# Kernel optimization log

Hardware: AMD Instinct MI355X
Metric: run time of the kernel (lower is better)

Reference implementation:

```python
import jax, jax.numpy as jnp
import numpy as np

N = 50000      # nodes
E = 800000     # edges
F_IN = 64      # n_features
H = 128        # graph_hidden_layers
LAT = 128      # latent_size
DH = 1024      # dense_hidden_layers
G = 256        # num graphs in batch
EPS = 1e-5


def setup_inputs() -> dict:
    key = jax.random.key(0)
    ks = jax.random.split(key, 32)
    def rn(k, shape, scale=0.05):
        return jax.random.normal(k, shape, dtype=jnp.float32) * scale
    inp = {
        "x": jax.random.normal(ks[0], (N, F_IN), dtype=jnp.float32),
        "origin": jax.random.normal(ks[1], (G, 3), dtype=jnp.float32),
        "direction": jax.random.normal(ks[2], (G, 3), dtype=jnp.float32),
        "edge_index": jax.random.randint(ks[3], (2, E), 0, N, dtype=jnp.int32),
        "batch": jnp.sort(jax.random.randint(ks[4], (N,), 0, G, dtype=jnp.int32)),
        # GCNConv weights
        "W1": rn(ks[5], (F_IN, H)), "b1": jnp.zeros((H,), jnp.float32),
        "W2": rn(ks[6], (H, H)),    "b2": jnp.zeros((H,), jnp.float32),
        "W3": rn(ks[7], (H, LAT)), "b3": jnp.zeros((LAT,), jnp.float32),
        # BatchNorm affine params
        "g1": jnp.ones((H,), jnp.float32),   "be1": jnp.zeros((H,), jnp.float32),
        "g2": jnp.ones((H,), jnp.float32),   "be2": jnp.zeros((H,), jnp.float32),
        "g3": jnp.ones((LAT,), jnp.float32), "be3": jnp.zeros((LAT,), jnp.float32),
        # Dense head: (LAT+6)->DH, then n_dense_layers=2 of DH->DH, then DH->3
        "Wd0": rn(ks[8], (LAT + 6, DH)), "bd0": jnp.zeros((DH,), jnp.float32),
        "Wd1": rn(ks[9], (DH, DH)),      "bd1": jnp.zeros((DH,), jnp.float32),
        "Wd2": rn(ks[10], (DH, DH)),     "bd2": jnp.zeros((DH,), jnp.float32),
        "Wout": rn(ks[11], (DH, 3)),     "bout": jnp.zeros((3,), jnp.float32),
    }
    return inp


def _gcn_conv(x, W, b, src, dst, deg_inv_sqrt):
    """PyG GCNConv with self-loops: D^{-1/2} (A+I) D^{-1/2} x W + b."""
    xW = x @ W  # [N, out]
    norm = deg_inv_sqrt[src] * deg_inv_sqrt[dst]  # [E]
    msg = xW[src] * norm[:, None]                 # gather + scale
    agg = jax.ops.segment_sum(msg, dst, num_segments=N)
    agg = agg + xW * (deg_inv_sqrt * deg_inv_sqrt)[:, None]  # self-loop term
    return agg + b


def _batchnorm(x, gamma, beta):
    m = jnp.mean(x, axis=0)
    v = jnp.mean(jnp.square(x - m), axis=0)
    return (x - m) * jax.lax.rsqrt(v + EPS) * gamma + beta


def reference(x, origin, direction, edge_index, batch,
              W1, b1, W2, b2, W3, b3,
              g1, be1, g2, be2, g3, be3,
              Wd0, bd0, Wd1, bd1, Wd2, bd2, Wout, bout):
    src, dst = edge_index[0], edge_index[1]
    # degree with self-loops (in-degree at dst, matching gcn_norm)
    deg = jax.ops.segment_sum(jnp.ones((E,), jnp.float32), dst, num_segments=N) + 1.0
    deg_inv_sqrt = jax.lax.rsqrt(deg)

    h = jax.nn.relu(_batchnorm(_gcn_conv(x, W1, b1, src, dst, deg_inv_sqrt), g1, be1))
    h = jax.nn.relu(_batchnorm(_gcn_conv(h, W2, b2, src, dst, deg_inv_sqrt), g2, be2))
    h = _batchnorm(_gcn_conv(h, W3, b3, src, dst, deg_inv_sqrt), g3, be3)

    # global mean pool over graphs
    sums = jax.ops.segment_sum(h, batch, num_segments=G)
    cnt = jax.ops.segment_sum(jnp.ones((N,), jnp.float32), batch, num_segments=G)
    pooled = sums / jnp.maximum(cnt, 1.0)[:, None]  # [G, LAT]

    z = jnp.concatenate([pooled, origin, direction], axis=1)  # [G, LAT+6]
    z = jax.nn.relu(z @ Wd0 + bd0)
    z = jax.nn.relu(z @ Wd1 + bd1)
    z = jax.nn.relu(z @ Wd2 + bd2)
    return z @ Wout + bout  # [G, 3]
```

## Files before the change

kernel.cpp:

```cpp
#include <hip/hip_runtime.h>

#define HC 128
#define FIN 64
#define DHID 1024
#define ZK 134
#define ZKP 160
#define NSCAT 4

typedef __attribute__((ext_vector_type(8))) short short8;
typedef __attribute__((ext_vector_type(8))) __bf16 bf16x8;
typedef __attribute__((ext_vector_type(4))) float f32x4;
typedef __attribute__((ext_vector_type(8))) unsigned short u16x8;
typedef __attribute__((ext_vector_type(4))) unsigned short u16x4;

union FragU { short8 s; bf16x8 b; u16x8 u; };

__device__ inline unsigned short rne_bf16(float x) {
    union { float f; unsigned u; } v; v.f = x;
    unsigned u = v.u;
    unsigned r = (u + 0x7fffu + ((u >> 16) & 1u)) >> 16;
    return (unsigned short)r;
}
__device__ inline float bf16_to_f(unsigned short h) {
    union { unsigned u; float f; } v; v.u = ((unsigned)h) << 16;
    return v.f;
}

__global__ void k_deg_i(const int* __restrict__ dst, int* __restrict__ cnt, int E) {
    int i = blockIdx.x * blockDim.x + threadIdx.x;
    if (i < E) atomicAdd(&cnt[dst[i]], 1);
}

__global__ void k_xtobf(const float* __restrict__ x, unsigned short* __restrict__ xb, int n4) {
    int i = blockIdx.x * blockDim.x + threadIdx.x;
    if (i >= n4) return;
    float4 v = ((const float4*)x)[i];
    u16x4 o;
    o[0] = rne_bf16(v.x); o[1] = rne_bf16(v.y);
    o[2] = rne_bf16(v.z); o[3] = rne_bf16(v.w);
    ((u16x4*)xb)[i] = o;
}

__global__ void k_scan1(const int* __restrict__ cnt, int* __restrict__ part,
                        int* __restrict__ bsum, float* __restrict__ dinv, int N) {
    __shared__ int sh[256];
    int t = threadIdx.x, i = blockIdx.x * 256 + t;
    int v = (i < N) ? cnt[i] : 0;
    if (i < N) dinv[i] = rsqrtf((float)v + 1.0f);
    sh[t] = v; __syncthreads();
    #pragma unroll
    for (int off = 1; off < 256; off <<= 1) {
        int tv = (t >= off) ? sh[t - off] : 0;
        __syncthreads();
        sh[t] += tv;
        __syncthreads();
    }
    if (i < N) part[i] = sh[t] - v;
    if (t == 255) bsum[blockIdx.x] = sh[255];
}

__global__ void k_scan2(int* __restrict__ bsum, int nb) {
    __shared__ int sh[256];
    int t = threadIdx.x;
    int v = (t < nb) ? bsum[t] : 0;
    sh[t] = v; __syncthreads();
    #pragma unroll
    for (int off = 1; off < 256; off <<= 1) {
        int tv = (t >= off) ? sh[t - off] : 0;
        __syncthreads();
        sh[t] += tv;
        __syncthreads();
    }
    if (t < nb) bsum[t] = sh[t] - v;
}

__global__ void k_scan3(const int* __restrict__ part, const int* __restrict__ bsum,
                        int* __restrict__ row_start, int* __restrict__ cur, int N) {
    int i = blockIdx.x * 256 + threadIdx.x;
    if (i < N) { int v = part[i] + bsum[blockIdx.x]; row_start[i] = v; cur[i] = v; }
}

__global__ void k_scatter2(const int* __restrict__ src, const int* __restrict__ dst,
                           const float* __restrict__ dinv,
                           int* __restrict__ cur, int2* __restrict__ csr,
                           int E, int rangeSize) {
    int e = blockIdx.x * blockDim.x + threadIdx.x;
    if (e >= E) return;
    int d = dst[e];
    int lo = blockIdx.y * rangeSize;
    if (d < lo || d >= lo + rangeSize) return;
    int s = src[e];
    int pos = atomicAdd(&cur[d], 1);
    int2 pk; pk.x = s; pk.y = __float_as_int(dinv[s] * dinv[d]);
    csr[pos] = pk;
}

template <int RF> struct BVec;
template <> struct BVec<64>  { using T = u16x4; static const int VPL = 4; };
template <> struct BVec<128> { using T = u16x8; static const int VPL = 8; };

template <int RF>
__global__ __launch_bounds__(256) void k_gather2b(const unsigned short* __restrict__ T,
                                                  const int2* __restrict__ csr,
                                                  const int* __restrict__ row_start,
                                                  const int* __restrict__ cnt,
                                                  const float* __restrict__ dinv,
                                                  unsigned short* __restrict__ agg, int N) {
    using vec = typename BVec<RF>::T;
    constexpr int VPL = BVec<RF>::VPL;
    int tid = threadIdx.x;
    int node = blockIdx.x * 16 + (tid >> 4);
    int q = tid & 15;
    if (node >= N) return;
    int beg = row_start[node];
    int end = beg + cnt[node];
    float d = dinv[node];
    vec sv = ((const vec*)(T + (size_t)node * RF))[q];
    float acc[VPL];
    #pragma unroll
    for (int i = 0; i < VPL; ++i) acc[i] = bf16_to_f(sv[i]) * d * d;
    int j = beg;
    for (; j + 8 <= end; j += 8) {
        int2 e[8];
        #pragma unroll
        for (int u = 0; u < 8; ++u) e[u] = csr[j + u];
        vec v[8];
        #pragma unroll
        for (int u = 0; u < 8; ++u) v[u] = ((const vec*)(T + (size_t)e[u].x * RF))[q];
        #pragma unroll
        for (int u = 0; u < 8; ++u) {
            float nn = __int_as_float(e[u].y);
            #pragma unroll
            for (int i = 0; i < VPL; ++i) acc[i] += bf16_to_f(v[u][i]) * nn;
        }
    }
    for (; j + 2 <= end; j += 2) {
        int2 e0 = csr[j], e1 = csr[j + 1];
        vec v0 = ((const vec*)(T + (size_t)e0.x * RF))[q];
        vec v1 = ((const vec*)(T + (size_t)e1.x * RF))[q];
        float n0 = __int_as_float(e0.y), n1 = __int_as_float(e1.y);
        #pragma unroll
        for (int i = 0; i < VPL; ++i)
            acc[i] += bf16_to_f(v0[i]) * n0 + bf16_to_f(v1[i]) * n1;
    }
    if (j < end) {
        int2 e0 = csr[j];
        vec v0 = ((const vec*)(T + (size_t)e0.x * RF))[q];
        float n0 = __int_as_float(e0.y);
        #pragma unroll
        for (int i = 0; i < VPL; ++i) acc[i] += bf16_to_f(v0[i]) * n0;
    }
    vec o;
    #pragma unroll
    for (int i = 0; i < VPL; ++i) o[i] = rne_bf16(acc[i]);
    ((vec*)(agg + (size_t)node * RF))[q] = o;
}

__global__ __launch_bounds__(256) void k_bn_reduce3(const unsigned short* __restrict__ x,
                                                    float* __restrict__ stat, int N) {
    int cg = threadIdx.x & 15;
    int rr = threadIdx.x >> 4;
    int rpb = (N + gridDim.x - 1) / gridDim.x;
    int r0 = blockIdx.x * rpb;
    int r1 = min(N, r0 + rpb);
    float s0=0.f,s1=0.f,s2=0.f,s3=0.f,s4=0.f,s5=0.f,s6=0.f,s7=0.f;
    float q0=0.f,q1=0.f,q2=0.f,q3=0.f,q4=0.f,q5=0.f,q6=0.f,q7=0.f;
    for (int r = r0 + rr; r < r1; r += 16) {
        u16x8 v = *(const u16x8*)(x + (size_t)r * HC + cg * 8);
        float f;
        f = bf16_to_f(v[0]); s0 += f; q0 += f * f;
        f = bf16_to_f(v[1]); s1 += f; q1 += f * f;
        f = bf16_to_f(v[2]); s2 += f; q2 += f * f;
        f = bf16_to_f(v[3]); s3 += f; q3 += f * f;
        f = bf16_to_f(v[4]); s4 += f; q4 += f * f;
        f = bf16_to_f(v[5]); s5 += f; q5 += f * f;
        f = bf16_to_f(v[6]); s6 += f; q6 += f * f;
        f = bf16_to_f(v[7]); s7 += f; q7 += f * f;
    }
    __shared__ float sh[16][136];
    int c0 = cg * 8;
    int tid = threadIdx.x;
    sh[rr][c0+0]=s0; sh[rr][c0+1]=s1; sh[rr][c0+2]=s2; sh[rr][c0+3]=s3;
    sh[rr][c0+4]=s4; sh[rr][c0+5]=s5; sh[rr][c0+6]=s6; sh[rr][c0+7]=s7;
    __syncthreads();
    if (tid < HC) {
        float tot = 0.f;
        #pragma unroll
        for (int r2 = 0; r2 < 16; ++r2) tot += sh[r2][tid];
        atomicAdd(&stat[tid], tot);
    }
    __syncthreads();
    sh[rr][c0+0]=q0; sh[rr][c0+1]=q1; sh[rr][c0+2]=q2; sh[rr][c0+3]=q3;
    sh[rr][c0+4]=q4; sh[rr][c0+5]=q5; sh[rr][c0+6]=q6; sh[rr][c0+7]=q7;
    __syncthreads();
    if (tid < HC) {
        float tot = 0.f;
        #pragma unroll
        for (int r2 = 0; r2 < 16; ++r2) tot += sh[r2][tid];
        atomicAdd(&stat[HC + tid], tot);
    }
}

__global__ void k_bn_apply3(unsigned short* __restrict__ t, const float* __restrict__ stat,
                            const float* __restrict__ gam, const float* __restrict__ bet,
                            float invN, int total8) {
    int i = blockIdx.x * blockDim.x + threadIdx.x;
    if (i >= total8) return;
    int k0 = (i * 8) & (HC - 1);
    u16x8 v = ((const u16x8*)t)[i];
    u16x8 o;
    #pragma unroll
    for (int j = 0; j < 8; ++j) {
        int k = k0 + j;
        float m = stat[k] * invN;
        float var = stat[HC + k] * invN - m * m;
        float istd = rsqrtf(var + 1e-5f);
        float sc = gam[k] * istd;
        float sh = bet[k] - m * sc;
        o[j] = rne_bf16(fmaxf(bf16_to_f(v[j]) * sc + sh, 0.f));
    }
    ((u16x8*)t)[i] = o;
}

__global__ void k_pool(const unsigned short* __restrict__ h, const int* __restrict__ batch,
                       const float* __restrict__ stat, const float* __restrict__ gam,
                       const float* __restrict__ bet, float invN,
                       float* __restrict__ pooled, float* __restrict__ cnt, int N) {
    int t = threadIdx.x;
    float m = stat[t] * invN;
    float var = stat[HC + t] * invN - m * m;
    float istd = rsqrtf(var + 1e-5f);
    float scv = gam[t] * istd;
    float shv = bet[t] - m * scv;
    int rpb = (N + gridDim.x - 1) / gridDim.x;
    int r0 = blockIdx.x * rpb;
    int r1 = min(N, r0 + rpb);
    if (r0 >= r1) return;
    int curb = batch[r0];
    float acc = 0.f; float c = 0.f;
    for (int r = r0; r < r1; ++r) {
        int b = batch[r];
        if (b != curb) {
            atomicAdd(&pooled[curb * HC + t], acc);
            if (t == 0) atomicAdd(&cnt[curb], c);
            curb = b; acc = 0.f; c = 0.f;
        }
        acc += bf16_to_f(h[(size_t)r * HC + t]) * scv + shv;
        c += 1.f;
    }
    atomicAdd(&pooled[curb * HC + t], acc);
    if (t == 0) atomicAdd(&cnt[curb], c);
}

__global__ void k_build_z(const float* __restrict__ pooled, const float* __restrict__ cnt,
                          const float* __restrict__ origin, const float* __restrict__ dir,
                          float* __restrict__ z, int G) {
    int g = blockIdx.x;
    int t = threadIdx.x;
    if (t >= ZKP) return;
    float v = 0.f;
    if (t < HC) {
        float c = fmaxf(cnt[g], 1.0f);
        v = pooled[g * HC + t] / c;
    } else if (t < HC + 3) {
        v = origin[g * 3 + (t - HC)];
    } else if (t < HC + 6) {
        v = dir[g * 3 + (t - HC - 3)];
    }
    z[g * ZKP + t] = v;
}

__global__ void k_wprep_all(const float* __restrict__ W1, const float* __restrict__ W2,
                            const float* __restrict__ W3,
                            unsigned short* __restrict__ w1h, unsigned short* __restrict__ w1l,
                            unsigned short* __restrict__ w2h, unsigned short* __restrict__ w2l,
                            unsigned short* __restrict__ w3h, unsigned short* __restrict__ w3l) {
    int i = blockIdx.x * blockDim.x + threadIdx.x;
    const float* W; unsigned short *th, *tl; int K, idx;
    if (i < FIN * HC)           { W = W1; th = w1h; tl = w1l; K = FIN; idx = i; }
    else if (i < FIN*HC + HC*HC){ W = W2; th = w2h; tl = w2l; K = HC;  idx = i - FIN*HC; }
    else if (i < FIN*HC + 2*HC*HC){ W = W3; th = w3h; tl = w3l; K = HC; idx = i - FIN*HC - HC*HC; }
    else return;
    int k = idx >> 7, n = idx & (HC - 1);
    float w = W[idx];
    unsigned short h = rne_bf16(w);
    th[n * K + k] = h;
    tl[n * K + k] = rne_bf16(w - bf16_to_f(h));
}

__global__ __launch_bounds__(256) void k_wprep2(const float* __restrict__ W,
                                                unsigned short* __restrict__ th,
                                                unsigned short* __restrict__ tl,
                                                int K, int KP, int NC) {
    __shared__ float tile[32][33];
    int kt = blockIdx.x * 32, nt = blockIdx.y * 32;
    int tx = threadIdx.x & 31, ty0 = threadIdx.x >> 5;
    #pragma unroll
    for (int i = 0; i < 4; ++i) {
        int ty = ty0 + i * 8;
        int k = kt + ty;
        float v = (k < K) ? W[(size_t)k * NC + nt + tx] : 0.f;
        tile[ty][tx] = v;
    }
    __syncthreads();
    #pragma unroll
    for (int i = 0; i < 4; ++i) {
        int ty = ty0 + i * 8;
        int n = nt + ty;
        int k = kt + tx;
        float w = tile[tx][ty];
        unsigned short h = rne_bf16(w);
        th[(size_t)n * KP + k] = h;
        tl[(size_t)n * KP + k] = rne_bf16(w - bf16_to_f(h));
    }
}

template <int KK>
__global__ __launch_bounds__(512) void gemm_node2(const unsigned short* __restrict__ A,
                                                  const unsigned short* __restrict__ wth,
                                                  const unsigned short* __restrict__ wtl,
                                                  unsigned short* __restrict__ C, int M) {
    constexpr int KS = KK / 32;
    int tid = threadIdx.x;
    int lane = tid & 63, wid = tid >> 6;
    int rw = wid & 1, cg = wid >> 1;
    int l15 = lane & 15, l4 = lane >> 4;
    int cbase = cg * 32;

    FragU bh[2][KS], bl[2][KS];
    #pragma unroll
    for (int ct = 0; ct < 2; ++ct) {
        int n = cbase + ct * 16 + l15;
        #pragma unroll
        for (int ks = 0; ks < KS; ++ks) {
            int k = ks * 32 + l4 * 8;
            bh[ct][ks].s = *(const short8*)(wth + (size_t)n * KK + k);
            bl[ct][ks].s = *(const short8*)(wtl + (size_t)n * KK + k);
        }
    }

    #pragma unroll
    for (int rt = 0; rt < 2; ++rt) {
        int m0 = blockIdx.x * 64 + rt * 32 + rw * 16;
        if (m0 < M) {
            int arow = min(m0 + l15, M - 1);
            f32x4 zero = {0.f, 0.f, 0.f, 0.f};
            f32x4 acc[2] = {zero, zero};
            #pragma unroll
            for (int ks = 0; ks < KS; ++ks) {
                int k0 = ks * 32 + l4 * 8;
                FragU a;
                a.u = *(const u16x8*)(A + (size_t)arow * KK + k0);
                #pragma unroll
                for (int ct = 0; ct < 2; ++ct) {
                    acc[ct] = __builtin_amdgcn_mfma_f32_16x16x32_bf16(a.b, bh[ct][ks].b, acc[ct], 0, 0, 0);
                    acc[ct] = __builtin_amdgcn_mfma_f32_16x16x32_bf16(a.b, bl[ct][ks].b, acc[ct], 0, 0, 0);
                }
            }
            #pragma unroll
            for (int ct = 0; ct < 2; ++ct) {
                int col = cbase + ct * 16 + l15;
                #pragma unroll
                for (int r = 0; r < 4; ++r) {
                    int row = m0 + l4 * 4 + r;
                    if (row < M)
                        C[(size_t)row * HC + col] = rne_bf16(acc[ct][r]);
                }
            }
        }
    }
}

__global__ __launch_bounds__(256) void gemm_head_sk(const float* __restrict__ A,
                                                    const unsigned short* __restrict__ wth,
                                                    const unsigned short* __restrict__ wtl,
                                                    float* __restrict__ Cpart,
                                                    int M, int N, int K, int slice) {
    int tid = threadIdx.x;
    int lane = tid & 63, wid = tid >> 6;
    int rw = wid & 1, cw = wid >> 1;
    int l15 = lane & 15, l4 = lane >> 4;
    int m0 = blockIdx.y * 32 + rw * 16;
    int cb = blockIdx.x * 64 + cw * 32;
    int z = blockIdx.z;
    int kbeg = z * slice;
    int kend = min(K, kbeg + slice);
    if (m0 >= M) return;

    int arow = m0 + l15;
    f32x4 zero = {0.f, 0.f, 0.f, 0.f};
    f32x4 acc[2] = {zero, zero};

    for (int k0 = kbeg; k0 < kend; k0 += 32) {
        int ka = k0 + l4 * 8;
        const float4 p0 = *(const float4*)(A + (size_t)arow * K + ka);
        const float4 p1 = *(const float4*)(A + (size_t)arow * K + ka + 4);
        float av[8] = {p0.x, p0.y, p0.z, p0.w, p1.x, p1.y, p1.z, p1.w};
        FragU ah, al;
        #pragma unroll
        for (int i = 0; i < 8; ++i) {
            unsigned short h = rne_bf16(av[i]);
            ah.s[i] = (short)h;
            al.s[i] = (short)rne_bf16(av[i] - bf16_to_f(h));
        }
        #pragma unroll
        for (int ct = 0; ct < 2; ++ct) {
            int n = cb + ct * 16 + l15;
            FragU bh, bl;
            bh.s = *(const short8*)(wth + (size_t)n * K + ka);
            bl.s = *(const short8*)(wtl + (size_t)n * K + ka);
            acc[ct] = __builtin_amdgcn_mfma_f32_16x16x32_bf16(ah.b, bh.b, acc[ct], 0, 0, 0);
            acc[ct] = __builtin_amdgcn_mfma_f32_16x16x32_bf16(ah.b, bl.b, acc[ct], 0, 0, 0);
            acc[ct] = __builtin_amdgcn_mfma_f32_16x16x32_bf16(al.b, bh.b, acc[ct], 0, 0, 0);
        }
    }

    float* Cz = Cpart + (size_t)z * M * N;
    #pragma unroll
    for (int ct = 0; ct < 2; ++ct) {
        int col = cb + ct * 16 + l15;
        #pragma unroll
        for (int r = 0; r < 4; ++r) {
            int row = m0 + l4 * 4 + r;
            Cz[(size_t)row * N + col] = acc[ct][r];
        }
    }
}

__global__ void k_reduce_br(const float* __restrict__ part, const float* __restrict__ bias,
                            float* __restrict__ C, int MN, int Nmask, int NZ) {
    int i = (blockIdx.x * blockDim.x + threadIdx.x) * 4;
    if (i >= MN) return;
    float4 acc = *(const float4*)(part + i);
    for (int zz = 1; zz < NZ; ++zz) {
        float4 p = *(const float4*)(part + (size_t)zz * MN + i);
        acc.x += p.x; acc.y += p.y; acc.z += p.z; acc.w += p.w;
    }
    int n = i & Nmask;
    acc.x += bias[n]; acc.y += bias[n + 1]; acc.z += bias[n + 2]; acc.w += bias[n + 3];
    acc.x = fmaxf(acc.x, 0.f); acc.y = fmaxf(acc.y, 0.f);
    acc.z = fmaxf(acc.z, 0.f); acc.w = fmaxf(acc.w, 0.f);
    *(float4*)(C + i) = acc;
}

__global__ void k_dense_out(const float* __restrict__ z, const float* __restrict__ W,
                            const float* __restrict__ b, float* __restrict__ out, int K) {
    int g = blockIdx.x;
    const float* zr = z + (size_t)g * K;
    float a0 = 0.f, a1 = 0.f, a2 = 0.f;
    for (int k = threadIdx.x; k < K; k += blockDim.x) {
        float zv = zr[k];
        a0 += zv * W[k * 3 + 0];
        a1 += zv * W[k * 3 + 1];
        a2 += zv * W[k * 3 + 2];
    }
    __shared__ float s[768];
    s[threadIdx.x] = a0; s[256 + threadIdx.x] = a1; s[512 + threadIdx.x] = a2;
    __syncthreads();
    for (int off = 128; off > 0; off >>= 1) {
        if ((int)threadIdx.x < off) {
            s[threadIdx.x]       += s[threadIdx.x + off];
            s[256 + threadIdx.x] += s[256 + threadIdx.x + off];
            s[512 + threadIdx.x] += s[512 + threadIdx.x + off];
        }
        __syncthreads();
    }
    if (threadIdx.x == 0) {
        out[g * 3 + 0] = s[0]   + b[0];
        out[g * 3 + 1] = s[256] + b[1];
        out[g * 3 + 2] = s[512] + b[2];
    }
}

extern "C" void kernel_launch(void* const* d_in, const int* in_sizes, int n_in,
                              void* d_out, int out_size, void* d_ws, size_t ws_size,
                              hipStream_t stream) {
    const float* x         = (const float*)d_in[0];
    const float* origin    = (const float*)d_in[1];
    const float* direction = (const float*)d_in[2];
    const int*   eidx      = (const int*)d_in[3];
    const int*   batch     = (const int*)d_in[4];
    const float* W1 = (const float*)d_in[5];
    const float* W2 = (const float*)d_in[7];
    const float* W3 = (const float*)d_in[9];
    const float* g1 = (const float*)d_in[11]; const float* be1 = (const float*)d_in[12];
    const float* g2 = (const float*)d_in[13]; const float* be2 = (const float*)d_in[14];
    const float* g3 = (const float*)d_in[15]; const float* be3 = (const float*)d_in[16];
    const float* Wd0 = (const float*)d_in[17]; const float* bd0 = (const float*)d_in[18];
    const float* Wd1 = (const float*)d_in[19]; const float* bd1 = (const float*)d_in[20];
    const float* Wd2 = (const float*)d_in[21]; const float* bd2 = (const float*)d_in[22];
    const float* Wout = (const float*)d_in[23]; const float* bout = (const float*)d_in[24];
    float* out = (float*)d_out;

    const int N = in_sizes[4];
    const int E = in_sizes[3] / 2;
    const int G = in_sizes[1] / 3;
    const int* src = eidx;
    const int* dst = eidx + E;

    char* ws = (char*)d_ws;
    size_t off = 0;
    auto alloc = [&](size_t nbytes) -> void* {
        void* p = (void*)(ws + off);
        off += (nbytes + 255) & ~(size_t)255;
        return p;
    };
    float* colstats = (float*)alloc(3 * 2 * HC * 4);
    float* pooled   = (float*)alloc((size_t)G * HC * 4);
    float* cntf     = (float*)alloc((size_t)G * 4);
    int*   degcnt   = (int*)alloc((size_t)N * 4);
    const size_t zeroBytes = 3 * 2 * HC * 4 + (size_t)G * HC * 4 + 1024  + (size_t)N * 4;

    float* dinv     = (float*)alloc((size_t)N * 4);
    int*   part     = (int*)alloc((size_t)N * 4);
    int*   bsum     = (int*)alloc(256 * 4);
    int*   row_start= (int*)alloc((size_t)N * 4);
    int*   cur      = (int*)alloc((size_t)N * 4);
    int2*  csr      = (int2*)alloc((size_t)E * 8);
    unsigned short* xb   = (unsigned short*)alloc((size_t)N * FIN * 2);
    unsigned short* aggx = (unsigned short*)alloc((size_t)N * FIN * 2);
    unsigned short* tabA = (unsigned short*)alloc((size_t)N * HC * 2);
    unsigned short* tabB = (unsigned short*)alloc((size_t)N * HC * 2);
    unsigned short* wt1h = (unsigned short*)alloc((size_t)FIN * HC * 2);
    unsigned short* wt1l = (unsigned short*)alloc((size_t)FIN * HC * 2);
    unsigned short* wt2h = (unsigned short*)alloc((size_t)HC * HC * 2);
    unsigned short* wt2l = (unsigned short*)alloc((size_t)HC * HC * 2);
    unsigned short* wt3h = (unsigned short*)alloc((size_t)HC * HC * 2);
    unsigned short* wt3l = (unsigned short*)alloc((size_t)HC * HC * 2);
    unsigned short* wd0h = (unsigned short*)alloc((size_t)DHID * ZKP * 2);
    unsigned short* wd0l = (unsigned short*)alloc((size_t)DHID * ZKP * 2);
    unsigned short* wd1h = (unsigned short*)alloc((size_t)DHID * DHID * 2);
    unsigned short* wd1l = (unsigned short*)alloc((size_t)DHID * DHID * 2);
    unsigned short* wd2h = (unsigned short*)alloc((size_t)DHID * DHID * 2);
    unsigned short* wd2l = (unsigned short*)alloc((size_t)DHID * DHID * 2);
    float* zbuf     = (float*)alloc((size_t)G * ZKP * 4);
    float* t0       = (float*)alloc((size_t)G * DHID * 4);
    float* t1       = (float*)alloc((size_t)G * DHID * 4);
    float* kpart    = (float*)alloc((size_t)8 * G * DHID * 4);
    (void)ws_size;

    const int nScanBlk = (N + 255) / 256;
    const int gemmBlk = (N + 63) / 64;
    const int gatherBlk = (N + 15) / 16;
    const int total8 = N * HC / 8;
    const float invN = 1.0f / (float)N;
    const int rangeSize = (N + NSCAT - 1) / NSCAT;

    hipMemsetAsync(colstats, 0, zeroBytes, stream);

    k_xtobf<<<(N * FIN / 4 + 255) / 256, 256, 0, stream>>>(x, xb, N * FIN / 4);
    k_wprep_all<<<(FIN * HC + 2 * HC * HC + 255) / 256, 256, 0, stream>>>(
        W1, W2, W3, wt1h, wt1l, wt2h, wt2l, wt3h, wt3l);
    k_wprep2<<<dim3(ZKP / 32, DHID / 32), 256, 0, stream>>>(Wd0, wd0h, wd0l, ZK, ZKP, DHID);
    k_wprep2<<<dim3(DHID / 32, DHID / 32), 256, 0, stream>>>(Wd1, wd1h, wd1l, DHID, DHID, DHID);
    k_wprep2<<<dim3(DHID / 32, DHID / 32), 256, 0, stream>>>(Wd2, wd2h, wd2l, DHID, DHID, DHID);

    k_deg_i<<<(E + 255) / 256, 256, 0, stream>>>(dst, degcnt, E);
    k_scan1<<<nScanBlk, 256, 0, stream>>>(degcnt, part, bsum, dinv, N);
    k_scan2<<<1, 256, 0, stream>>>(bsum, nScanBlk);
    k_scan3<<<nScanBlk, 256, 0, stream>>>(part, bsum, row_start, cur, N);
    k_scatter2<<<dim3((E + 255) / 256, NSCAT), 256, 0, stream>>>(src, dst, dinv, cur, csr,
                                                                 E, rangeSize);

    k_gather2b<FIN><<<gatherBlk, 256, 0, stream>>>(xb, csr, row_start, degcnt, dinv, aggx, N);
    gemm_node2<FIN><<<gemmBlk, 512, 0, stream>>>(aggx, wt1h, wt1l, tabA, N);
    k_bn_reduce3<<<256, 256, 0, stream>>>(tabA, colstats + 0 * 2 * HC, N);

    k_bn_apply3<<<(total8 + 255) / 256, 256, 0, stream>>>(tabA, colstats + 0 * 2 * HC,
                                                          g1, be1, invN, total8);
    gemm_node2<HC><<<gemmBlk, 512, 0, stream>>>(tabA, wt2h, wt2l, tabB, N);
    k_gather2b<HC><<<gatherBlk, 256, 0, stream>>>(tabB, csr, row_start, degcnt, dinv, tabA, N);
    k_bn_reduce3<<<256, 256, 0, stream>>>(tabA, colstats + 1 * 2 * HC, N);

    k_bn_apply3<<<(total8 + 255) / 256, 256, 0, stream>>>(tabA, colstats + 1 * 2 * HC,
                                                          g2, be2, invN, total8);
    gemm_node2<HC><<<gemmBlk, 512, 0, stream>>>(tabA, wt3h, wt3l, tabB, N);
    k_gather2b<HC><<<gatherBlk, 256, 0, stream>>>(tabB, csr, row_start, degcnt, dinv, tabA, N);
    k_bn_reduce3<<<256, 256, 0, stream>>>(tabA, colstats + 2 * 2 * HC, N);

    k_pool<<<512, HC, 0, stream>>>(tabA, batch, colstats + 2 * 2 * HC, g3, be3, invN,
                                   pooled, cntf, N);
    k_build_z<<<G, 192, 0, stream>>>(pooled, cntf, origin, direction, zbuf, G);

    const int MN = G * DHID;
    const int rblk = (MN / 4 + 255) / 256;

    gemm_head_sk<<<dim3(DHID / 64, (G + 31) / 32, 5), 256, 0, stream>>>(
        zbuf, wd0h, wd0l, kpart, G, DHID, ZKP, 32);
    k_reduce_br<<<rblk, 256, 0, stream>>>(kpart, bd0, t0, MN, DHID - 1, 5);

    gemm_head_sk<<<dim3(DHID / 64, (G + 31) / 32, 8), 256, 0, stream>>>(
        t0, wd1h, wd1l, kpart, G, DHID, DHID, 128);
    k_reduce_br<<<rblk, 256, 0, stream>>>(kpart, bd1, t1, MN, DHID - 1, 8);

    gemm_head_sk<<<dim3(DHID / 64, (G + 31) / 32, 8), 256, 0, stream>>>(
        t1, wd2h, wd2l, kpart, G, DHID, DHID, 128);
    k_reduce_br<<<rblk, 256, 0, stream>>>(kpart, bd2, t0, MN, DHID - 1, 8);

    k_dense_out<<<G, 256, 0, stream>>>(t0, Wout, bout, out, DHID);
}
```

Baseline: 404.7 us.

## Factor GCN normalization into pre/post row scaling and build CSR via atomic ranks

The symmetric normalization D^-1/2 A D^-1/2 is factored so source rows are pre-scaled by dinv (in the bf16 conversion of x or the GEMM epilogue) and the aggregated sum is scaled by dinv[dst] once. This lets the CSR store only the source index (4 bytes instead of 8) and makes the gather a plain unweighted sum. The CSR build records each edge's atomic rank during degree counting and scatters deterministically, replacing the four-pass range-filtered atomic scatter. Rounding the pre-scaled values to bf16 before the sum changes numerics slightly.

```diff
diff --git a/kernel.cpp b/kernel.cpp
--- a/kernel.cpp
+++ b/kernel.cpp
@@ -5,7 +5,6 @@
 #define DHID 1024
 #define ZK 134
 #define ZKP 160
-#define NSCAT 4
 
 typedef __attribute__((ext_vector_type(8))) short short8;
 typedef __attribute__((ext_vector_type(8))) __bf16 bf16x8;
@@ -26,18 +25,21 @@
     return v.f;
 }
 
-__global__ void k_deg_i(const int* __restrict__ dst, int* __restrict__ cnt, int E) {
+__global__ void k_deg_rank(const int* __restrict__ dst, int* __restrict__ cnt,
+                           int* __restrict__ rank, int E) {
     int i = blockIdx.x * blockDim.x + threadIdx.x;
-    if (i < E) atomicAdd(&cnt[dst[i]], 1);
-}
-
-__global__ void k_xtobf(const float* __restrict__ x, unsigned short* __restrict__ xb, int n4) {
+    if (i < E) rank[i] = atomicAdd(&cnt[dst[i]], 1);
+}
+
+__global__ void k_xtobf(const float* __restrict__ x, const float* __restrict__ dinv,
+                        unsigned short* __restrict__ xb, int n4) {
     int i = blockIdx.x * blockDim.x + threadIdx.x;
     if (i >= n4) return;
+    float d = dinv[i / (FIN / 4)];
     float4 v = ((const float4*)x)[i];
     u16x4 o;
-    o[0] = rne_bf16(v.x); o[1] = rne_bf16(v.y);
-    o[2] = rne_bf16(v.z); o[3] = rne_bf16(v.w);
+    o[0] = rne_bf16(v.x * d); o[1] = rne_bf16(v.y * d);
+    o[2] = rne_bf16(v.z * d); o[3] = rne_bf16(v.w * d);
     ((u16x4*)xb)[i] = o;
 }
 
@@ -75,24 +77,18 @@
 }
 
 __global__ void k_scan3(const int* __restrict__ part, const int* __restrict__ bsum,
-                        int* __restrict__ row_start, int* __restrict__ cur, int N) {
+                        int* __restrict__ row_start, int N) {
     int i = blockIdx.x * 256 + threadIdx.x;
-    if (i < N) { int v = part[i] + bsum[blockIdx.x]; row_start[i] = v; cur[i] = v; }
-}
-
-__global__ void k_scatter2(const int* __restrict__ src, const int* __restrict__ dst,
-                           const float* __restrict__ dinv,
-                           int* __restrict__ cur, int2* __restrict__ csr,
-                           int E, int rangeSize) {
+    if (i < N) row_start[i] = part[i] + bsum[blockIdx.x];
+}
+
+__global__ void k_scatter3(const int* __restrict__ src, const int* __restrict__ dst,
+                           const int* __restrict__ rank, const int* __restrict__ row_start,
+                           int* __restrict__ csr, int E) {
     int e = blockIdx.x * blockDim.x + threadIdx.x;
     if (e >= E) return;
     int d = dst[e];
-    int lo = blockIdx.y * rangeSize;
-    if (d < lo || d >= lo + rangeSize) return;
-    int s = src[e];
-    int pos = atomicAdd(&cur[d], 1);
-    int2 pk; pk.x = s; pk.y = __float_as_int(dinv[s] * dinv[d]);
-    csr[pos] = pk;
+    csr[row_start[d] + rank[e]] = src[e];
 }
 
 template <int RF> struct BVec;
@@ -100,12 +96,12 @@
 template <> struct BVec<128> { using T = u16x8; static const int VPL = 8; };
 
 template <int RF>
-__global__ __launch_bounds__(256) void k_gather2b(const unsigned short* __restrict__ T,
-                                                  const int2* __restrict__ csr,
-                                                  const int* __restrict__ row_start,
-                                                  const int* __restrict__ cnt,
-                                                  const float* __restrict__ dinv,
-                                                  unsigned short* __restrict__ agg, int N) {
+__global__ __launch_bounds__(256) void k_gather3(const unsigned short* __restrict__ T,
+                                                 const int* __restrict__ csr,
+                                                 const int* __restrict__ row_start,
+                                                 const int* __restrict__ cnt,
+                                                 const float* __restrict__ dinv,
+                                                 unsigned short* __restrict__ agg, int N) {
     using vec = typename BVec<RF>::T;
     constexpr int VPL = BVec<RF>::VPL;
     int tid = threadIdx.x;
@@ -118,41 +114,44 @@
     vec sv = ((const vec*)(T + (size_t)node * RF))[q];
     float acc[VPL];
     #pragma unroll
-    for (int i = 0; i < VPL; ++i) acc[i] = bf16_to_f(sv[i]) * d * d;
+    for (int i = 0; i < VPL; ++i) acc[i] = bf16_to_f(sv[i]);
     int j = beg;
     for (; j + 8 <= end; j += 8) {
-        int2 e[8];
-        #pragma unroll
-        for (int u = 0; u < 8; ++u) e[u] = csr[j + u];
-        vec v[8];
-        #pragma unroll
-        for (int u = 0; u < 8; ++u) v[u] = ((const vec*)(T + (size_t)e[u].x * RF))[q];
-        #pragma unroll
-        for (int u = 0; u < 8; ++u) {
-            float nn = __int_as_float(e[u].y);
-            #pragma unroll
-            for (int i = 0; i < VPL; ++i) acc[i] += bf16_to_f(v[u][i]) * nn;
+        int e0 = csr[j], e1 = csr[j+1], e2 = csr[j+2], e3 = csr[j+3];
+        int e4 = csr[j+4], e5 = csr[j+5], e6 = csr[j+6], e7 = csr[j+7];
+        vec v0 = ((const vec*)(T + (size_t)e0 * RF))[q];
+        vec v1 = ((const vec*)(T + (size_t)e1 * RF))[q];
+        vec v2 = ((const vec*)(T + (size_t)e2 * RF))[q];
+        vec v3 = ((const vec*)(T + (size_t)e3 * RF))[q];
+        vec v4 = ((const vec*)(T + (size_t)e4 * RF))[q];
+        vec v5 = ((const vec*)(T + (size_t)e5 * RF))[q];
+        vec v6 = ((const vec*)(T + (size_t)e6 * RF))[q];
+        vec v7 = ((const vec*)(T + (size_t)e7 * RF))[q];
+        #pragma unroll
+        for (int i = 0; i < VPL; ++i) {
+            acc[i] += (bf16_to_f(v0[i]) + bf16_to_f(v1[i]))
+                    + (bf16_to_f(v2[i]) + bf16_to_f(v3[i]))
+                    + (bf16_to_f(v4[i]) + bf16_to_f(v5[i]))
+                    + (bf16_to_f(v6[i]) + bf16_to_f(v7[i]));
         }
     }
     for (; j + 2 <= end; j += 2) {
-        int2 e0 = csr[j], e1 = csr[j + 1];
-        vec v0 = ((const vec*)(T + (size_t)e0.x * RF))[q];
-        vec v1 = ((const vec*)(T + (size_t)e1.x * RF))[q];
-        float n0 = __int_as_float(e0.y), n1 = __int_as_float(e1.y);
+        int e0 = csr[j], e1 = csr[j + 1];
+        vec v0 = ((const vec*)(T + (size_t)e0 * RF))[q];
+        vec v1 = ((const vec*)(T + (size_t)e1 * RF))[q];
         #pragma unroll
         for (int i = 0; i < VPL; ++i)
-            acc[i] += bf16_to_f(v0[i]) * n0 + bf16_to_f(v1[i]) * n1;
+            acc[i] += bf16_to_f(v0[i]) + bf16_to_f(v1[i]);
     }
     if (j < end) {
-        int2 e0 = csr[j];
-        vec v0 = ((const vec*)(T + (size_t)e0.x * RF))[q];
-        float n0 = __int_as_float(e0.y);
-        #pragma unroll
-        for (int i = 0; i < VPL; ++i) acc[i] += bf16_to_f(v0[i]) * n0;
+        int e0 = csr[j];
+        vec v0 = ((const vec*)(T + (size_t)e0 * RF))[q];
+        #pragma unroll
+        for (int i = 0; i < VPL; ++i) acc[i] += bf16_to_f(v0[i]);
     }
     vec o;
     #pragma unroll
-    for (int i = 0; i < VPL; ++i) o[i] = rne_bf16(acc[i]);
+    for (int i = 0; i < VPL; ++i) o[i] = rne_bf16(acc[i] * d);
     ((vec*)(agg + (size_t)node * RF))[q] = o;
 }
 
@@ -315,10 +314,11 @@
     }
 }
 
-template <int KK>
+template <int KK, bool SCALE>
 __global__ __launch_bounds__(512) void gemm_node2(const unsigned short* __restrict__ A,
                                                   const unsigned short* __restrict__ wth,
                                                   const unsigned short* __restrict__ wtl,
+                                                  const float* __restrict__ dinv,
                                                   unsigned short* __restrict__ C, int M) {
     constexpr int KS = KK / 32;
     int tid = threadIdx.x;
@@ -357,14 +357,25 @@
                     acc[ct] = __builtin_amdgcn_mfma_f32_16x16x32_bf16(a.b, bl[ct][ks].b, acc[ct], 0, 0, 0);
                 }
             }
+            float dv0 = 1.f, dv1 = 1.f, dv2 = 1.f, dv3 = 1.f;
+            if (SCALE) {
+                int rbase = m0 + l4 * 4;
+                dv0 = dinv[min(rbase + 0, M - 1)];
+                dv1 = dinv[min(rbase + 1, M - 1)];
+                dv2 = dinv[min(rbase + 2, M - 1)];
+                dv3 = dinv[min(rbase + 3, M - 1)];
+            }
             #pragma unroll
             for (int ct = 0; ct < 2; ++ct) {
                 int col = cbase + ct * 16 + l15;
                 #pragma unroll
                 for (int r = 0; r < 4; ++r) {
                     int row = m0 + l4 * 4 + r;
-                    if (row < M)
-                        C[(size_t)row * HC + col] = rne_bf16(acc[ct][r]);
+                    if (row < M) {
+                        float v = acc[ct][r];
+                        if (SCALE) v *= (r == 0 ? dv0 : r == 1 ? dv1 : r == 2 ? dv2 : dv3);
+                        C[(size_t)row * HC + col] = rne_bf16(v);
+                    }
                 }
             }
         }
@@ -515,8 +526,8 @@
     int*   part     = (int*)alloc((size_t)N * 4);
     int*   bsum     = (int*)alloc(256 * 4);
     int*   row_start= (int*)alloc((size_t)N * 4);
-    int*   cur      = (int*)alloc((size_t)N * 4);
-    int2*  csr      = (int2*)alloc((size_t)E * 8);
+    int*   rank     = (int*)alloc((size_t)E * 4);
+    int*   csr      = (int*)alloc((size_t)E * 4);
     unsigned short* xb   = (unsigned short*)alloc((size_t)N * FIN * 2);
     unsigned short* aggx = (unsigned short*)alloc((size_t)N * FIN * 2);
     unsigned short* tabA = (unsigned short*)alloc((size_t)N * HC * 2);
@@ -544,38 +555,37 @@
     const int gatherBlk = (N + 15) / 16;
     const int total8 = N * HC / 8;
     const float invN = 1.0f / (float)N;
-    const int rangeSize = (N + NSCAT - 1) / NSCAT;
 
     hipMemsetAsync(colstats, 0, zeroBytes, stream);
 
-    k_xtobf<<<(N * FIN / 4 + 255) / 256, 256, 0, stream>>>(x, xb, N * FIN / 4);
     k_wprep_all<<<(FIN * HC + 2 * HC * HC + 255) / 256, 256, 0, stream>>>(
         W1, W2, W3, wt1h, wt1l, wt2h, wt2l, wt3h, wt3l);
     k_wprep2<<<dim3(ZKP / 32, DHID / 32), 256, 0, stream>>>(Wd0, wd0h, wd0l, ZK, ZKP, DHID);
     k_wprep2<<<dim3(DHID / 32, DHID / 32), 256, 0, stream>>>(Wd1, wd1h, wd1l, DHID, DHID, DHID);
     k_wprep2<<<dim3(DHID / 32, DHID / 32), 256, 0, stream>>>(Wd2, wd2h, wd2l, DHID, DHID, DHID);
 
-    k_deg_i<<<(E + 255) / 256, 256, 0, stream>>>(dst, degcnt, E);
+    k_deg_rank<<<(E + 255) / 256, 256, 0, stream>>>(dst, degcnt, rank, E);
     k_scan1<<<nScanBlk, 256, 0, stream>>>(degcnt, part, bsum, dinv, N);
     k_scan2<<<1, 256, 0, stream>>>(bsum, nScanBlk);
-    k_scan3<<<nScanBlk, 256, 0, stream>>>(part, bsum, row_start, cur, N);
-    k_scatter2<<<dim3((E + 255) / 256, NSCAT), 256, 0, stream>>>(src, dst, dinv, cur, csr,
-                                                                 E, rangeSize);
-
-    k_gather2b<FIN><<<gatherBlk, 256, 0, stream>>>(xb, csr, row_start, degcnt, dinv, aggx, N);
-    gemm_node2<FIN><<<gemmBlk, 512, 0, stream>>>(aggx, wt1h, wt1l, tabA, N);
+    k_scan3<<<nScanBlk, 256, 0, stream>>>(part, bsum, row_start, N);
+    k_scatter3<<<(E + 255) / 256, 256, 0, stream>>>(src, dst, rank, row_start, csr, E);
+
+    k_xtobf<<<(N * FIN / 4 + 255) / 256, 256, 0, stream>>>(x, dinv, xb, N * FIN / 4);
+
+    k_gather3<FIN><<<gatherBlk, 256, 0, stream>>>(xb, csr, row_start, degcnt, dinv, aggx, N);
+    gemm_node2<FIN, false><<<gemmBlk, 512, 0, stream>>>(aggx, wt1h, wt1l, nullptr, tabA, N);
     k_bn_reduce3<<<256, 256, 0, stream>>>(tabA, colstats + 0 * 2 * HC, N);
 
     k_bn_apply3<<<(total8 + 255) / 256, 256, 0, stream>>>(tabA, colstats + 0 * 2 * HC,
                                                           g1, be1, invN, total8);
-    gemm_node2<HC><<<gemmBlk, 512, 0, stream>>>(tabA, wt2h, wt2l, tabB, N);
-    k_gather2b<HC><<<gatherBlk, 256, 0, stream>>>(tabB, csr, row_start, degcnt, dinv, tabA, N);
+    gemm_node2<HC, true><<<gemmBlk, 512, 0, stream>>>(tabA, wt2h, wt2l, dinv, tabB, N);
+    k_gather3<HC><<<gatherBlk, 256, 0, stream>>>(tabB, csr, row_start, degcnt, dinv, tabA, N);
     k_bn_reduce3<<<256, 256, 0, stream>>>(tabA, colstats + 1 * 2 * HC, N);
 
     k_bn_apply3<<<(total8 + 255) / 256, 256, 0, stream>>>(tabA, colstats + 1 * 2 * HC,
                                                           g2, be2, invN, total8);
-    gemm_node2<HC><<<gemmBlk, 512, 0, stream>>>(tabA, wt3h, wt3l, tabB, N);
-    k_gather2b<HC><<<gatherBlk, 256, 0, stream>>>(tabB, csr, row_start, degcnt, dinv, tabA, N);
+    gemm_node2<HC, true><<<gemmBlk, 512, 0, stream>>>(tabA, wt3h, wt3l, dinv, tabB, N);
+    k_gather3<HC><<<gatherBlk, 256, 0, stream>>>(tabB, csr, row_start, degcnt, dinv, tabA, N);
     k_bn_reduce3<<<256, 256, 0, stream>>>(tabA, colstats + 2 * 2 * HC, N);
 
     k_pool<<<512, HC, 0, stream>>>(tabA, batch, colstats + 2 * 2 * HC, g3, be3, invN,
```

Measured after the change: 367.7 us. -9.1%, faster.
